# Optimization experiments

Measured on AMD Instinct MI355X. Metric: run time of the kernel, lower is better.

The kernel has to match this reference:

```python
import jax, jax.numpy as jnp
import numpy as np

N = 100000      # nodes
E = 1600000     # edges (avg degree 16)
F_IN = 14       # Mutagenicity num_node_features
H = 64          # hidden_channels
C = 2           # Mutagenicity num_classes
G = 512         # graphs in batch


def setup_inputs() -> dict:
    key = jax.random.key(0)
    ks = jax.random.split(key, 16)
    x = jax.random.normal(ks[0], (N, F_IN), jnp.float32)
    edge_index = jax.random.randint(ks[1], (2, E), 0, N, dtype=jnp.int32)
    batch = jnp.sort(jax.random.randint(ks[2], (N,), 0, G, dtype=jnp.int32))
    def lin(k, fi, fo):
        bound = 1.0 / np.sqrt(fi)
        kw, kb = jax.random.split(k)
        W = jax.random.uniform(kw, (fi, fo), jnp.float32, -bound, bound)
        b = jax.random.uniform(kb, (fo,), jnp.float32, -bound, bound)
        return W, b
    W1, b1 = lin(ks[3], F_IN, H)
    W2, b2 = lin(ks[4], H, H)
    W3, b3 = lin(ks[5], H, H)
    W4, b4 = lin(ks[6], H, H)
    W5, b5 = lin(ks[7], H, H)
    Wlin, blin = lin(ks[8], H, C)
    return {"x": x, "W1": W1, "b1": b1, "W2": W2, "b2": b2, "W3": W3, "b3": b3,
            "W4": W4, "b4": b4, "W5": W5, "b5": b5, "Wlin": Wlin, "blin": blin,
            "edge_index": edge_index, "batch": batch}


def _gcn_conv(h, W, b, src, dst, norm, dinv):
    # PyG GCNConv: out = D^{-1/2}(A+I)D^{-1/2} (h W) + b
    m = h @ W                                              # [N, Fout]
    agg = jax.ops.segment_sum(m[src] * norm[:, None], dst, num_segments=N)
    agg = agg + m * dinv[:, None]                          # self-loop term (norm = 1/deg)
    return agg + b


def reference(x, W1, b1, W2, b2, W3, b3, W4, b4, W5, b5, Wlin, blin, edge_index, batch):
    src, dst = edge_index[0], edge_index[1]
    # degree with self-loops (counted on target nodes, source_to_target flow)
    deg = jax.ops.segment_sum(jnp.ones(E, jnp.float32), dst, num_segments=N) + 1.0
    dinv_sqrt = jax.lax.rsqrt(deg)
    norm = dinv_sqrt[src] * dinv_sqrt[dst]                 # per-edge weight
    dinv = dinv_sqrt * dinv_sqrt                           # self-loop weight 1/deg

    h = jax.nn.relu(_gcn_conv(x, W1, b1, src, dst, norm, dinv))
    h = jax.nn.relu(_gcn_conv(h, W2, b2, src, dst, norm, dinv))
    h = jax.nn.relu(_gcn_conv(h, W3, b3, src, dst, norm, dinv))
    h = jax.nn.relu(_gcn_conv(h, W4, b4, src, dst, norm, dinv))
    h = jax.nn.relu(_gcn_conv(h, W5, b5, src, dst, norm, dinv))

    pooled = jax.ops.segment_max(h, batch, num_segments=G)  # [G, H]
    return pooled @ Wlin + blin                             # [G, C]
```

## Files before the change

kernel.cpp:

```cpp
#include <hip/hip_runtime.h>
#include <hip/hip_bf16.h>


#define HDIM 64
#define SCAN_CHUNK 1024
#define FILL_S 8


__global__ __launch_bounds__(256) void count_sharded(const int* __restrict__ dst,
                                                     int* __restrict__ deg,
                                                     int E, int shard_w, int nchunks) {
    int shard = blockIdx.x & (FILL_S - 1);
    int chunk = blockIdx.x >> 3;
    int epc = (E + nchunks - 1) / nchunks;
    int e0 = chunk * epc;
    int e1 = min(e0 + epc, E);
    int lo = shard * shard_w, hi = lo + shard_w;
    for (int e = e0 + (int)threadIdx.x; e < e1; e += 256) {
        int d = dst[e];
        if (d >= lo && d < hi) atomicAdd(&deg[d], 1);
    }
}

__global__ __launch_bounds__(256) void partial_sums(const int* __restrict__ deg,
                                                    int* __restrict__ psum, int n) {
    __shared__ int red[256];
    int base = blockIdx.x * SCAN_CHUNK;
    int s = 0;
    #pragma unroll
    for (int j = 0; j < 4; ++j) {
        int i = base + j * 256 + threadIdx.x;
        if (i < n) s += deg[i];
    }
    red[threadIdx.x] = s;
    __syncthreads();
    for (int off = 128; off > 0; off >>= 1) {
        if (threadIdx.x < off) red[threadIdx.x] += red[threadIdx.x + off];
        __syncthreads();
    }
    if (threadIdx.x == 0) psum[blockIdx.x] = red[0];
}

__global__ __launch_bounds__(128) void scan_partials(int* __restrict__ psum, int nb) {
    __shared__ int tmp[128];
    int t = threadIdx.x;
    int v = (t < nb) ? psum[t] : 0;
    tmp[t] = v;
    __syncthreads();
    for (int off = 1; off < 128; off <<= 1) {
        int u = (t >= off) ? tmp[t - off] : 0;
        __syncthreads();
        tmp[t] += u;
        __syncthreads();
    }
    if (t < nb) psum[t] = tmp[t] - v;
}

__global__ __launch_bounds__(256) void scan_final(const int* __restrict__ deg,
                                                  const int* __restrict__ psum,
                                                  int* __restrict__ rowptr, int n) {
    __shared__ int ts[256];
    int t = threadIdx.x;
    int base = blockIdx.x * SCAN_CHUNK + t * 4;
    int v[4];
    int s = 0;
    #pragma unroll
    for (int j = 0; j < 4; ++j) {
        int i = base + j;
        v[j] = (i < n) ? deg[i] : 0;
        s += v[j];
    }
    ts[t] = s;
    __syncthreads();
    int mine = s;
    for (int off = 1; off < 256; off <<= 1) {
        int u = (t >= off) ? ts[t - off] : 0;
        __syncthreads();
        ts[t] += u;
        __syncthreads();
    }
    int ex = ts[t] - mine + psum[blockIdx.x];
    #pragma unroll
    for (int j = 0; j < 4; ++j) {
        int i = base + j;
        if (i < n) rowptr[i] = ex;
        ex += v[j];
    }
}

__global__ __launch_bounds__(256) void node_prep(const int* __restrict__ deg,
                                                 const int* __restrict__ rowptr,
                                                 const float* __restrict__ x,
                                                 float* __restrict__ ds,
                                                 int* __restrict__ cursor,
                                                 float* __restrict__ xp, int n) {
    int i = blockIdx.x * blockDim.x + threadIdx.x;
    if (i >= n) return;
    float d = (float)(deg[i] + 1);
    float dsv = 1.0f / sqrtf(d);
    ds[i] = dsv;
    cursor[i] = rowptr[i];
    const float* xr = x + (size_t)i * 14;
    float* xo = xp + (size_t)i * 16;
    #pragma unroll
    for (int j = 0; j < 14; ++j) xo[j] = xr[j] * dsv;
    xo[14] = 0.0f;
    xo[15] = 0.0f;
}

__global__ __launch_bounds__(256) void fill_csr_sharded(const int* __restrict__ src,
                                                        const int* __restrict__ dst,
                                                        int* __restrict__ cursor,
                                                        int* __restrict__ csr_src,
                                                        int E, int shard_w, int nchunks) {
    int shard = blockIdx.x & (FILL_S - 1);
    int chunk = blockIdx.x >> 3;
    int epc = (E + nchunks - 1) / nchunks;
    int e0 = chunk * epc;
    int e1 = min(e0 + epc, E);
    int lo = shard * shard_w, hi = lo + shard_w;
    for (int e = e0 + (int)threadIdx.x; e < e1; e += 256) {
        int d = dst[e];
        if (d >= lo && d < hi) {
            int pos = atomicAdd(&cursor[d], 1);
            csr_src[pos] = src[e];
        }
    }
}


__global__ __launch_bounds__(256) void gather16(const float* __restrict__ xp,
                                               const int* __restrict__ rowptr,
                                               const int* __restrict__ cnt,
                                               const int* __restrict__ csr_src,
                                               const float* __restrict__ ds,
                                               float* __restrict__ agg16, int n_nodes) {
    int lane = threadIdx.x & 63;
    int sub = lane >> 4, l = lane & 15;
    int wave = blockIdx.x * (blockDim.x >> 6) + (threadIdx.x >> 6);
    int node = wave * 4 + sub;
    if (node >= n_nodes) return;
    float dsn = ds[node];
    float a0 = xp[node * 16 + l];
    float a1 = 0.f, a2 = 0.f, a3 = 0.f;
    int s = rowptr[node];
    int e = s + cnt[node];
    int i = s;
    for (; i + 3 < e; i += 4) {
        int s0 = csr_src[i], s1 = csr_src[i + 1], s2 = csr_src[i + 2], s3 = csr_src[i + 3];
        a0 += xp[s0 * 16 + l];
        a1 += xp[s1 * 16 + l];
        a2 += xp[s2 * 16 + l];
        a3 += xp[s3 * 16 + l];
    }
    for (; i < e; ++i) a0 += xp[csr_src[i] * 16 + l];
    agg16[node * 16 + l] = ((a0 + a1) + (a2 + a3)) * dsn;
}


template <int K, int KW, bool BIAS_RELU, bool SCALE>
__global__ __launch_bounds__(256) void matmul_k(const float* __restrict__ h,
                                                const float* __restrict__ W,
                                                const float* __restrict__ bias,
                                                const float* __restrict__ ds,
                                                float* __restrict__ m, int n_nodes) {
    __shared__ float Wl[K * HDIM];
    __shared__ float ldsbuf[4 * 4 * K];
    int t = threadIdx.x;
    {
        const float4* Wg4 = reinterpret_cast<const float4*>(W);
        float4* Wl4 = reinterpret_cast<float4*>(Wl);
        const int NF4 = K * HDIM / 4;
        #pragma unroll
        for (int f = t; f < NF4; f += 256) {
            int k = f >> 4;
            float4 v;
            if (k < KW) v = Wg4[f];
            else        v = make_float4(0.f, 0.f, 0.f, 0.f);
            Wl4[f] = v;
        }
    }
    __syncthreads();

    int lane = t & 63;
    int wv = t >> 6;
    int wave = blockIdx.x * 4 + wv;
    int n0 = wave * 4;
    if (n0 >= n_nodes) return;
    float bl = BIAS_RELU ? bias[lane] : 0.f;

    if (n0 + 3 < n_nodes) {
        float* myl = &ldsbuf[wv * 4 * K];
        const float4* src4 = reinterpret_cast<const float4*>(h + (size_t)n0 * K);
        if constexpr (K == 64) {
            reinterpret_cast<float4*>(myl)[lane] = src4[lane];
        } else {
            if (lane < K) reinterpret_cast<float4*>(myl)[lane] = src4[lane];
        }
        const float4* r0 = reinterpret_cast<const float4*>(myl + 0 * K);
        const float4* r1 = reinterpret_cast<const float4*>(myl + 1 * K);
        const float4* r2 = reinterpret_cast<const float4*>(myl + 2 * K);
        const float4* r3 = reinterpret_cast<const float4*>(myl + 3 * K);
        float a0[4] = {0, 0, 0, 0}, a1[4] = {0, 0, 0, 0};
        float a2[4] = {0, 0, 0, 0}, a3[4] = {0, 0, 0, 0};
        #pragma unroll
        for (int k4 = 0; k4 < K / 4; ++k4) {
            int c = k4 & 3;
            float4 v0 = r0[k4], v1 = r1[k4], v2 = r2[k4], v3 = r3[k4];
            float w0 = Wl[(4 * k4 + 0) * HDIM + lane];
            float w1 = Wl[(4 * k4 + 1) * HDIM + lane];
            float w2 = Wl[(4 * k4 + 2) * HDIM + lane];
            float w3 = Wl[(4 * k4 + 3) * HDIM + lane];
            a0[c] += v0.x * w0 + v0.y * w1 + v0.z * w2 + v0.w * w3;
            a1[c] += v1.x * w0 + v1.y * w1 + v1.z * w2 + v1.w * w3;
            a2[c] += v2.x * w0 + v2.y * w1 + v2.z * w2 + v2.w * w3;
            a3[c] += v3.x * w0 + v3.y * w1 + v3.z * w2 + v3.w * w3;
        }
        float s0 = (a0[0] + a0[1]) + (a0[2] + a0[3]);
        float s1 = (a1[0] + a1[1]) + (a1[2] + a1[3]);
        float s2 = (a2[0] + a2[1]) + (a2[2] + a2[3]);
        float s3 = (a3[0] + a3[1]) + (a3[2] + a3[3]);
        if constexpr (BIAS_RELU) {
            s0 = fmaxf(s0 + bl, 0.f);
            s1 = fmaxf(s1 + bl, 0.f);
            s2 = fmaxf(s2 + bl, 0.f);
            s3 = fmaxf(s3 + bl, 0.f);
        }
        if constexpr (SCALE) {
            s0 *= ds[n0 + 0];
            s1 *= ds[n0 + 1];
            s2 *= ds[n0 + 2];
            s3 *= ds[n0 + 3];
        }
        m[(size_t)(n0 + 0) * HDIM + lane] = s0;
        m[(size_t)(n0 + 1) * HDIM + lane] = s1;
        m[(size_t)(n0 + 2) * HDIM + lane] = s2;
        m[(size_t)(n0 + 3) * HDIM + lane] = s3;
    } else {
        for (int n = n0; n < n_nodes; ++n) {
            const float4* hrow = reinterpret_cast<const float4*>(h + (size_t)n * K);
            float acc[4] = {0, 0, 0, 0};
            #pragma unroll
            for (int k4 = 0; k4 < K / 4; ++k4) {
                float4 hv = hrow[k4];
                acc[k4 & 3] += hv.x * Wl[(4 * k4 + 0) * HDIM + lane] +
                               hv.y * Wl[(4 * k4 + 1) * HDIM + lane] +
                               hv.z * Wl[(4 * k4 + 2) * HDIM + lane] +
                               hv.w * Wl[(4 * k4 + 3) * HDIM + lane];
            }
            float s = (acc[0] + acc[1]) + (acc[2] + acc[3]);
            if constexpr (BIAS_RELU) s = fmaxf(s + bl, 0.f);
            if constexpr (SCALE) s *= ds[n];
            m[(size_t)n * HDIM + lane] = s;
        }
    }
}


__global__ __launch_bounds__(256) void gcn_gather(const float* __restrict__ m,
                                                  const int* __restrict__ rowptr,
                                                  const int* __restrict__ cnt,
                                                  const int* __restrict__ csr_src,
                                                  const float* __restrict__ ds,
                                                  const float* __restrict__ bias,
                                                  float* __restrict__ hout, int n_nodes) {
    int lane = threadIdx.x & 63;
    int node = blockIdx.x * (blockDim.x >> 6) + (threadIdx.x >> 6);
    if (node >= n_nodes) return;
    float dsn = ds[node];
    float a0 = m[node * HDIM + lane];
    float a1 = 0.f, a2 = 0.f, a3 = 0.f;
    float a4 = 0.f, a5 = 0.f, a6 = 0.f, a7 = 0.f;
    int s = rowptr[node];
    int e = s + cnt[node];
    int i = s;
    for (; i + 15 < e; i += 16) {
        int t0 = csr_src[i],      t1 = csr_src[i + 1],  t2 = csr_src[i + 2],  t3 = csr_src[i + 3];
        int t4 = csr_src[i + 4],  t5 = csr_src[i + 5],  t6 = csr_src[i + 6],  t7 = csr_src[i + 7];
        int t8 = csr_src[i + 8],  t9 = csr_src[i + 9],  ta = csr_src[i + 10], tb = csr_src[i + 11];
        int tc = csr_src[i + 12], td = csr_src[i + 13], te = csr_src[i + 14], tf = csr_src[i + 15];
        a0 += m[t0 * HDIM + lane];
        a1 += m[t1 * HDIM + lane];
        a2 += m[t2 * HDIM + lane];
        a3 += m[t3 * HDIM + lane];
        a4 += m[t4 * HDIM + lane];
        a5 += m[t5 * HDIM + lane];
        a6 += m[t6 * HDIM + lane];
        a7 += m[t7 * HDIM + lane];
        a0 += m[t8 * HDIM + lane];
        a1 += m[t9 * HDIM + lane];
        a2 += m[ta * HDIM + lane];
        a3 += m[tb * HDIM + lane];
        a4 += m[tc * HDIM + lane];
        a5 += m[td * HDIM + lane];
        a6 += m[te * HDIM + lane];
        a7 += m[tf * HDIM + lane];
    }
    for (; i + 7 < e; i += 8) {
        int t0 = csr_src[i],     t1 = csr_src[i + 1], t2 = csr_src[i + 2], t3 = csr_src[i + 3];
        int t4 = csr_src[i + 4], t5 = csr_src[i + 5], t6 = csr_src[i + 6], t7 = csr_src[i + 7];
        a0 += m[t0 * HDIM + lane];
        a1 += m[t1 * HDIM + lane];
        a2 += m[t2 * HDIM + lane];
        a3 += m[t3 * HDIM + lane];
        a4 += m[t4 * HDIM + lane];
        a5 += m[t5 * HDIM + lane];
        a6 += m[t6 * HDIM + lane];
        a7 += m[t7 * HDIM + lane];
    }
    for (; i + 1 < e; i += 2) {
        int t0 = csr_src[i], t1 = csr_src[i + 1];
        a0 += m[t0 * HDIM + lane];
        a1 += m[t1 * HDIM + lane];
    }
    if (i < e) a0 += m[csr_src[i] * HDIM + lane];
    float v = ((a0 + a1) + (a2 + a3) + ((a4 + a5) + (a6 + a7))) * dsn + bias[lane];
    hout[node * HDIM + lane] = fmaxf(v, 0.f);
}


__global__ __launch_bounds__(256) void pool_linear(const float* __restrict__ h,
                                                   const int* __restrict__ batch,
                                                   const float* __restrict__ Wlin,
                                                   const float* __restrict__ blin,
                                                   float* __restrict__ out,
                                                   int n_nodes, int n_graphs) {
    int lane = threadIdx.x & 63;
    int g = blockIdx.x * (blockDim.x >> 6) + (threadIdx.x >> 6);
    if (g >= n_graphs) return;
    int lo = 0, hi = n_nodes;
    while (lo < hi) { int mid = (lo + hi) >> 1; if (batch[mid] < g) lo = mid + 1; else hi = mid; }
    int start = lo;
    hi = n_nodes;
    while (lo < hi) { int mid = (lo + hi) >> 1; if (batch[mid] < g + 1) lo = mid + 1; else hi = mid; }
    int end = lo;
    float vmax = 0.f;
    for (int n = start; n < end; ++n) vmax = fmaxf(vmax, h[(size_t)n * HDIM + lane]);
    float p0 = vmax * Wlin[lane * 2 + 0];
    float p1 = vmax * Wlin[lane * 2 + 1];
    #pragma unroll
    for (int off = 32; off > 0; off >>= 1) {
        p0 += __shfl_xor(p0, off);
        p1 += __shfl_xor(p1, off);
    }
    if (lane == 0) {
        out[g * 2 + 0] = p0 + blin[0];
        out[g * 2 + 1] = p1 + blin[1];
    }
}


extern "C" void kernel_launch(void* const* d_in, const int* in_sizes, int n_in,
                              void* d_out, int out_size, void* d_ws, size_t ws_size,
                              hipStream_t stream) {
    const float* x    = (const float*)d_in[0];
    const float* W1   = (const float*)d_in[1];
    const float* b1   = (const float*)d_in[2];
    const float* W2   = (const float*)d_in[3];
    const float* b2   = (const float*)d_in[4];
    const float* W3   = (const float*)d_in[5];
    const float* b3   = (const float*)d_in[6];
    const float* W4   = (const float*)d_in[7];
    const float* b4   = (const float*)d_in[8];
    const float* W5   = (const float*)d_in[9];
    const float* b5   = (const float*)d_in[10];
    const float* Wlin = (const float*)d_in[11];
    const float* blin = (const float*)d_in[12];
    const int* edge_index = (const int*)d_in[13];
    const int* batch      = (const int*)d_in[14];

    const int N = in_sizes[0] / 14;
    const int E = in_sizes[13] / 2;
    const int G = out_size / 2;
    const int* srcp = edge_index;
    const int* dstp = edge_index + E;

    char* ws = (char*)d_ws;
    size_t off = 0;
    auto alloc = [&](size_t bytes) -> void* {
        void* p = ws + off;
        off = (off + bytes + 255) & ~(size_t)255;
        return p;
    };
    int*   deg     = (int*)alloc((size_t)N * 4);
    int*   rowptr  = (int*)alloc((size_t)N * 4);
    int*   cursor  = (int*)alloc((size_t)N * 4);
    int*   psum    = (int*)alloc(128 * 4);
    float* ds      = (float*)alloc((size_t)N * 4);
    int*   csr_src = (int*)alloc((size_t)E * 4);
    float* buf_m   = (float*)alloc((size_t)N * HDIM * 4);
    float* buf_h   = (float*)alloc((size_t)N * HDIM * 4);
    (void)ws_size;
    float* xp    = buf_h;
    float* agg16 = buf_m;

    const int NB = (N + SCAN_CHUNK - 1) / SCAN_CHUNK;
    const int fill_chunks = 512;
    const int shard_w = (N + FILL_S - 1) / FILL_S;

    hipMemsetAsync(deg, 0, (size_t)N * 4, stream);
    count_sharded<<<fill_chunks * FILL_S, 256, 0, stream>>>(dstp, deg, E, shard_w, fill_chunks);
    partial_sums<<<NB, 256, 0, stream>>>(deg, psum, N);
    scan_partials<<<1, 128, 0, stream>>>(psum, NB);
    scan_final<<<NB, 256, 0, stream>>>(deg, psum, rowptr, N);
    node_prep<<<(N + 255) / 256, 256, 0, stream>>>(deg, rowptr, x, ds, cursor, xp, N);
    fill_csr_sharded<<<fill_chunks * FILL_S, 256, 0, stream>>>(srcp, dstp, cursor, csr_src,
                                                               E, shard_w, fill_chunks);

    const int gemm_blocks = (N + 15) / 16;
    const int gather_blocks = (N + 3) / 4;
    const int g16_blocks = (N + 15) / 16;

    gather16<<<g16_blocks, 256, 0, stream>>>(xp, rowptr, deg, csr_src, ds, agg16, N);
    matmul_k<16, 14, true, false><<<gemm_blocks, 256, 0, stream>>>(agg16, W1, b1, ds, buf_h, N);

    matmul_k<64, 64, false, true><<<gemm_blocks, 256, 0, stream>>>(buf_h, W2, b2, ds, buf_m, N);
    gcn_gather<<<gather_blocks, 256, 0, stream>>>(buf_m, rowptr, deg, csr_src, ds, b2, buf_h, N);
    matmul_k<64, 64, false, true><<<gemm_blocks, 256, 0, stream>>>(buf_h, W3, b3, ds, buf_m, N);
    gcn_gather<<<gather_blocks, 256, 0, stream>>>(buf_m, rowptr, deg, csr_src, ds, b3, buf_h, N);
    matmul_k<64, 64, false, true><<<gemm_blocks, 256, 0, stream>>>(buf_h, W4, b4, ds, buf_m, N);
    gcn_gather<<<gather_blocks, 256, 0, stream>>>(buf_m, rowptr, deg, csr_src, ds, b4, buf_h, N);
    matmul_k<64, 64, false, true><<<gemm_blocks, 256, 0, stream>>>(buf_h, W5, b5, ds, buf_m, N);
    gcn_gather<<<gather_blocks, 256, 0, stream>>>(buf_m, rowptr, deg, csr_src, ds, b5, buf_h, N);

    pool_linear<<<(G + 3) / 4, 256, 0, stream>>>(buf_h, batch, Wlin, blin, (float*)d_out, N, G);
}
```

Baseline: 712.5 us.

## Reorder GCN layers to aggregate-then-transform and fuse gather with matmul

Uses linearity to aggregate the pre-scaled hidden features first and then apply the 64x64 weight inside the same kernel, which is loaded into shared memory per block. Layer 1's matmul now emits scaled output, and the four separate matmul and gather launch pairs become four fused launches. This removes a full write and read of the N x 64 intermediate per layer and halves the number of launches. In exchange each 4-node block reloads the 16KB weight into LDS, and the per-node matvec runs through wave shuffles, which adds instruction work and LDS pressure that can lower occupancy.

```diff
diff --git a/kernel.cpp b/kernel.cpp
--- a/kernel.cpp
+++ b/kernel.cpp
@@ -257,18 +257,31 @@
 }
 
 
-__global__ __launch_bounds__(256) void gcn_gather(const float* __restrict__ m,
-                                                  const int* __restrict__ rowptr,
-                                                  const int* __restrict__ cnt,
-                                                  const int* __restrict__ csr_src,
-                                                  const float* __restrict__ ds,
-                                                  const float* __restrict__ bias,
-                                                  float* __restrict__ hout, int n_nodes) {
-    int lane = threadIdx.x & 63;
-    int node = blockIdx.x * (blockDim.x >> 6) + (threadIdx.x >> 6);
+template <bool SCALE_OUT>
+__global__ __launch_bounds__(256) void gcn_fused(const float* __restrict__ m,
+                                                 const int* __restrict__ rowptr,
+                                                 const int* __restrict__ cnt,
+                                                 const int* __restrict__ csr_src,
+                                                 const float* __restrict__ ds,
+                                                 const float* __restrict__ W,
+                                                 const float* __restrict__ bias,
+                                                 float* __restrict__ hout, int n_nodes) {
+    __shared__ float Wl[HDIM * HDIM];
+    int t = threadIdx.x;
+    {
+        const float4* Wg4 = reinterpret_cast<const float4*>(W);
+        float4* Wl4 = reinterpret_cast<float4*>(Wl);
+        #pragma unroll
+        for (int f = t; f < HDIM * HDIM / 4; f += 256) Wl4[f] = Wg4[f];
+    }
+    __syncthreads();
+
+    int lane = t & 63;
+    int node = blockIdx.x * 4 + (t >> 6);
     if (node >= n_nodes) return;
     float dsn = ds[node];
-    float a0 = m[node * HDIM + lane];
+
+    float a0 = m[(size_t)node * HDIM + lane];
     float a1 = 0.f, a2 = 0.f, a3 = 0.f;
     float a4 = 0.f, a5 = 0.f, a6 = 0.f, a7 = 0.f;
     int s = rowptr[node];
@@ -279,43 +292,54 @@
         int t4 = csr_src[i + 4],  t5 = csr_src[i + 5],  t6 = csr_src[i + 6],  t7 = csr_src[i + 7];
         int t8 = csr_src[i + 8],  t9 = csr_src[i + 9],  ta = csr_src[i + 10], tb = csr_src[i + 11];
         int tc = csr_src[i + 12], td = csr_src[i + 13], te = csr_src[i + 14], tf = csr_src[i + 15];
-        a0 += m[t0 * HDIM + lane];
-        a1 += m[t1 * HDIM + lane];
-        a2 += m[t2 * HDIM + lane];
-        a3 += m[t3 * HDIM + lane];
-        a4 += m[t4 * HDIM + lane];
-        a5 += m[t5 * HDIM + lane];
-        a6 += m[t6 * HDIM + lane];
-        a7 += m[t7 * HDIM + lane];
-        a0 += m[t8 * HDIM + lane];
-        a1 += m[t9 * HDIM + lane];
-        a2 += m[ta * HDIM + lane];
-        a3 += m[tb * HDIM + lane];
-        a4 += m[tc * HDIM + lane];
-        a5 += m[td * HDIM + lane];
-        a6 += m[te * HDIM + lane];
-        a7 += m[tf * HDIM + lane];
+        a0 += m[(size_t)t0 * HDIM + lane];
+        a1 += m[(size_t)t1 * HDIM + lane];
+        a2 += m[(size_t)t2 * HDIM + lane];
+        a3 += m[(size_t)t3 * HDIM + lane];
+        a4 += m[(size_t)t4 * HDIM + lane];
+        a5 += m[(size_t)t5 * HDIM + lane];
+        a6 += m[(size_t)t6 * HDIM + lane];
+        a7 += m[(size_t)t7 * HDIM + lane];
+        a0 += m[(size_t)t8 * HDIM + lane];
+        a1 += m[(size_t)t9 * HDIM + lane];
+        a2 += m[(size_t)ta * HDIM + lane];
+        a3 += m[(size_t)tb * HDIM + lane];
+        a4 += m[(size_t)tc * HDIM + lane];
+        a5 += m[(size_t)td * HDIM + lane];
+        a6 += m[(size_t)te * HDIM + lane];
+        a7 += m[(size_t)tf * HDIM + lane];
     }
     for (; i + 7 < e; i += 8) {
         int t0 = csr_src[i],     t1 = csr_src[i + 1], t2 = csr_src[i + 2], t3 = csr_src[i + 3];
         int t4 = csr_src[i + 4], t5 = csr_src[i + 5], t6 = csr_src[i + 6], t7 = csr_src[i + 7];
-        a0 += m[t0 * HDIM + lane];
-        a1 += m[t1 * HDIM + lane];
-        a2 += m[t2 * HDIM + lane];
-        a3 += m[t3 * HDIM + lane];
-        a4 += m[t4 * HDIM + lane];
-        a5 += m[t5 * HDIM + lane];
-        a6 += m[t6 * HDIM + lane];
-        a7 += m[t7 * HDIM + lane];
+        a0 += m[(size_t)t0 * HDIM + lane];
+        a1 += m[(size_t)t1 * HDIM + lane];
+        a2 += m[(size_t)t2 * HDIM + lane];
+        a3 += m[(size_t)t3 * HDIM + lane];
+        a4 += m[(size_t)t4 * HDIM + lane];
+        a5 += m[(size_t)t5 * HDIM + lane];
+        a6 += m[(size_t)t6 * HDIM + lane];
+        a7 += m[(size_t)t7 * HDIM + lane];
     }
     for (; i + 1 < e; i += 2) {
         int t0 = csr_src[i], t1 = csr_src[i + 1];
-        a0 += m[t0 * HDIM + lane];
-        a1 += m[t1 * HDIM + lane];
-    }
-    if (i < e) a0 += m[csr_src[i] * HDIM + lane];
-    float v = ((a0 + a1) + (a2 + a3) + ((a4 + a5) + (a6 + a7))) * dsn + bias[lane];
-    hout[node * HDIM + lane] = fmaxf(v, 0.f);
+        a0 += m[(size_t)t0 * HDIM + lane];
+        a1 += m[(size_t)t1 * HDIM + lane];
+    }
+    if (i < e) a0 += m[(size_t)csr_src[i] * HDIM + lane];
+    float a = (((a0 + a1) + (a2 + a3)) + ((a4 + a5) + (a6 + a7))) * dsn;
+
+    float o0 = bias[lane], o1 = 0.f, o2 = 0.f, o3 = 0.f;
+    #pragma unroll
+    for (int k = 0; k < 16; ++k) {
+        o0 += __shfl(a, 4 * k + 0) * Wl[(4 * k + 0) * HDIM + lane];
+        o1 += __shfl(a, 4 * k + 1) * Wl[(4 * k + 1) * HDIM + lane];
+        o2 += __shfl(a, 4 * k + 2) * Wl[(4 * k + 2) * HDIM + lane];
+        o3 += __shfl(a, 4 * k + 3) * Wl[(4 * k + 3) * HDIM + lane];
+    }
+    float o = fmaxf((o0 + o1) + (o2 + o3), 0.f);
+    if constexpr (SCALE_OUT) o *= dsn;
+    hout[(size_t)node * HDIM + lane] = o;
 }
 
 
@@ -408,20 +432,16 @@
                                                                E, shard_w, fill_chunks);
 
     const int gemm_blocks = (N + 15) / 16;
-    const int gather_blocks = (N + 3) / 4;
+    const int fused_blocks = (N + 3) / 4;
     const int g16_blocks = (N + 15) / 16;
 
     gather16<<<g16_blocks, 256, 0, stream>>>(xp, rowptr, deg, csr_src, ds, agg16, N);
-    matmul_k<16, 14, true, false><<<gemm_blocks, 256, 0, stream>>>(agg16, W1, b1, ds, buf_h, N);
-
-    matmul_k<64, 64, false, true><<<gemm_blocks, 256, 0, stream>>>(buf_h, W2, b2, ds, buf_m, N);
-    gcn_gather<<<gather_blocks, 256, 0, stream>>>(buf_m, rowptr, deg, csr_src, ds, b2, buf_h, N);
-    matmul_k<64, 64, false, true><<<gemm_blocks, 256, 0, stream>>>(buf_h, W3, b3, ds, buf_m, N);
-    gcn_gather<<<gather_blocks, 256, 0, stream>>>(buf_m, rowptr, deg, csr_src, ds, b3, buf_h, N);
-    matmul_k<64, 64, false, true><<<gemm_blocks, 256, 0, stream>>>(buf_h, W4, b4, ds, buf_m, N);
-    gcn_gather<<<gather_blocks, 256, 0, stream>>>(buf_m, rowptr, deg, csr_src, ds, b4, buf_h, N);
-    matmul_k<64, 64, false, true><<<gemm_blocks, 256, 0, stream>>>(buf_h, W5, b5, ds, buf_m, N);
-    gcn_gather<<<gather_blocks, 256, 0, stream>>>(buf_m, rowptr, deg, csr_src, ds, b5, buf_h, N);
+    matmul_k<16, 14, true, true><<<gemm_blocks, 256, 0, stream>>>(agg16, W1, b1, ds, buf_h, N);
+
+    gcn_fused<true ><<<fused_blocks, 256, 0, stream>>>(buf_h, rowptr, deg, csr_src, ds, W2, b2, buf_m, N);
+    gcn_fused<true ><<<fused_blocks, 256, 0, stream>>>(buf_m, rowptr, deg, csr_src, ds, W3, b3, buf_h, N);
+    gcn_fused<true ><<<fused_blocks, 256, 0, stream>>>(buf_h, rowptr, deg, csr_src, ds, W4, b4, buf_m, N);
+    gcn_fused<false><<<fused_blocks, 256, 0, stream>>>(buf_m, rowptr, deg, csr_src, ds, W5, b5, buf_h, N);
 
     pool_linear<<<(G + 3) / 4, 256, 0, stream>>>(buf_h, batch, Wlin, blin, (float*)d_out, N, G);
 }
```

Result: slower. 856.3 us (+20.2%).
